# Optimization experiments

Hardware: AMD Instinct MI355X
Metric: run time of the kernel (lower is better)

Reference implementation:

```python
import jax, jax.numpy as jnp
import numpy as np

T = 8          # temporal window (hardcoded '8' in the original)
N = 2048       # num_neurons
S = 8192       # num_synapses per neuron
MAXW = 8.0
UCAPTURE = 10.0 / 128.0
UMINUS = 10.0 / 128.0
USEARCH = 1.0 / 128.0
UBACKOFF = 96.0 / 128.0
UMIN = 4.0 / 128.0


def setup_inputs() -> dict:
    key = jax.random.key(0)
    k1, k2, k3 = jax.random.split(key, 3)
    all_input_spikes = jax.random.randint(k1, (T, N, S), 0, 2, dtype=jnp.int32)
    all_output_spikes = jax.random.randint(k2, (T, N), 0, 2, dtype=jnp.int32)
    W = jax.random.uniform(k3, (N, S), dtype=jnp.float32, minval=-0.5, maxval=8.5)
    return {"all_input_spikes": all_input_spikes,
            "all_output_spikes": all_output_spikes,
            "W": W}


def reference(all_input_spikes, all_output_spikes, W):
    # Clamp weights to [0, 8] (the two torch.where clamps).
    w = jnp.clip(W, 0.0, MAXW)  # [N, S]

    # Spike times encoded as 8 - (spike count over the temporal window).
    in_t = (8 - jnp.sum(all_input_spikes, axis=0)).astype(jnp.int32)        # [N, S]
    out_t = (8 - jnp.sum(all_output_spikes, axis=0)).astype(jnp.int32)[:, None]  # [N, 1]

    wn = w / MAXW
    p_plus = wn * (2.0 - wn)            # Bernoulli prob for fplus
    p_minus = (1.0 - wn) * (1.0 + wn)   # Bernoulli prob for fminus

    rk = jax.random.split(jax.random.key(42), 8)
    dt = w.dtype
    fplus = jax.random.bernoulli(rk[0], p_plus).astype(dt)
    fminus = jax.random.bernoulli(rk[1], p_minus).astype(dt)
    ucap = jax.random.bernoulli(rk[2], UCAPTURE, (N, S)).astype(dt)
    uminus = jax.random.bernoulli(rk[3], UMINUS, (N, S)).astype(dt)
    usearch = jax.random.bernoulli(rk[4], USEARCH, (N, S)).astype(dt)
    ubackoff = jax.random.bernoulli(rk[5], UBACKOFF, (N, S)).astype(dt)
    # umin is sampled independently in each of the four branches
    umin1 = jax.random.bernoulli(rk[6], UMIN, (N, S)).astype(dt)
    k7a, k7b, k7c = jax.random.split(rk[7], 3)
    umin2 = jax.random.bernoulli(k7a, UMIN, (N, S)).astype(dt)
    umin3 = jax.random.bernoulli(k7b, UMIN, (N, S)).astype(dt)
    umin4 = jax.random.bernoulli(k7c, UMIN, (N, S)).astype(dt)

    in_fired = in_t < 8
    out_fired = out_t < 8

    # Branch 1: capture (input at or before output)
    b1 = jnp.where(in_fired & out_fired & (in_t <= out_t),
                   w + ucap * jnp.maximum(fplus, umin1), w)
    # Branch 2: minus (input after output)
    b2 = jnp.where(in_fired & out_fired & (in_t > out_t),
                   b1 - uminus * jnp.maximum(fminus, umin2), b1)
    # Branch 3: search (input fired, output silent)
    b3 = jnp.where(in_fired & (out_t == 8),
                   b2 + usearch * jnp.maximum(fplus, umin3), b2)
    # Branch 4: backoff (input silent, output fired)
    b4 = jnp.where((in_t == 8) & out_fired,
                   b3 - ubackoff * jnp.maximum(fminus, umin4), b3)
    return b4
```

## Files before the change

kernel.cpp:

```cpp
#include <hip/hip_runtime.h>

#define TT 8
#define NN 2048
#define SS 8192
#define MM (NN * SS)

#define TH_CAP10  655360u
#define TH_SEARCH 65536u
#define TH_BACK   6291456u
#define TH_MIN    262144u

#define EPT       8
#define NBLOCKS   (MM / 256 / EPT)

typedef int   __attribute__((ext_vector_type(4))) intx4;
typedef float __attribute__((ext_vector_type(4))) floatx4;
typedef unsigned __attribute__((ext_vector_type(4))) uintx4;

struct Tbl { unsigned v[32]; };

__host__ __device__ __forceinline__ void tf2x32(unsigned k0, unsigned k1,
                                                unsigned x0, unsigned x1,
                                                unsigned& o0, unsigned& o1) {
  const unsigned ks2 = k0 ^ k1 ^ 0x1BD11BDAu;
  x0 += k0; x1 += k1;
#define TFR(r) { x0 += x1; x1 = (x1 << (r)) | (x1 >> (32 - (r))); x1 ^= x0; }
  TFR(13) TFR(15) TFR(26) TFR(6)
  x0 += k1;  x1 += ks2 + 1u;
  TFR(17) TFR(29) TFR(16) TFR(24)
  x0 += ks2; x1 += k0 + 2u;
  TFR(13) TFR(15) TFR(26) TFR(6)
  x0 += k0;  x1 += k1 + 3u;
  TFR(17) TFR(29) TFR(16) TFR(24)
  x0 += k1;  x1 += ks2 + 4u;
  TFR(13) TFR(15) TFR(26) TFR(6)
  x0 += ks2; x1 += k0 + 5u;
#undef TFR
  o0 = x0; o1 = x1;
}

__global__ __launch_bounds__(256) void ModSTDP_58823872086838_kernel(
    const int* __restrict__ inS,
    const int* __restrict__ outS,
    const float* __restrict__ W,
    float* __restrict__ out,
    Tbl tb)
{
  __shared__ __align__(16) unsigned tbl[32];
  if (threadIdx.x < 32) tbl[threadIdx.x] = tb.v[threadIdx.x];
  __syncthreads();

  const unsigned tid  = blockIdx.x * blockDim.x + threadIdx.x;
  const unsigned base = tid * EPT;
  const unsigned n    = base >> 13;

  int osum = 0;
#pragma unroll
  for (int t = 0; t < TT; ++t) osum += outS[t * NN + n];
  const bool outF = osum > 0;

  intx4 s[TT][2];
#pragma unroll
  for (int t = 0; t < TT; ++t) {
    const int* p = inS + (size_t)t * MM + base;
    s[t][0] = *reinterpret_cast<const intx4*>(p);
    s[t][1] = *reinterpret_cast<const intx4*>(p + 4);
  }
  const floatx4 w0 = *reinterpret_cast<const floatx4*>(W + base);
  const floatx4 w1 = *reinterpret_cast<const floatx4*>(W + base + 4);

  int cnt[EPT] = {0, 0, 0, 0, 0, 0, 0, 0};
#pragma unroll
  for (int t = 0; t < TT; ++t) {
#pragma unroll
    for (int e = 0; e < EPT; ++e) cnt[e] += s[t][e >> 2][e & 3];
  }

  float res[EPT];
#pragma unroll
  for (int e = 0; e < EPT; ++e) {
    const unsigned j = base + (unsigned)e;
    const float wraw = (e < 4) ? w0[e & 3] : w1[e & 3];
    const float w = fminf(fmaxf(wraw, 0.0f), 8.0f);
    const int c = cnt[e];
    const bool inF = c > 0;
    const bool active = inF | outF;
    const unsigned idx = inF ? (outF ? ((c >= osum) ? 0u : 1u) : 2u) : 3u;

    const uintx4 r0 = *reinterpret_cast<const uintx4*>(tbl + (idx << 3));
    const uintx4 r1 = *reinterpret_cast<const uintx4*>(tbl + (idx << 3) + 4);
    const unsigned ka0 = r0.x, ka1 = r0.y, kb0 = r0.z, kb1 = r0.w;
    const unsigned kc0 = r1.x, kc1 = r1.y, thB = r1.z;
    const float sgn = __uint_as_float(r1.w);

    const float wn = w * 0.125f;
    const float pp = __fmul_rn(wn, __fsub_rn(2.0f, wn));
    const float pm = __fmul_rn(__fsub_rn(1.0f, wn), __fadd_rn(1.0f, wn));
    const float pA = (idx & 1u) ? pm : pp;

    unsigned a0, a1, b0, b1, c0, c1;
    tf2x32(ka0, ka1, 0u, j, a0, a1);
    const unsigned bitsA = a0 ^ a1;
    const float u = __uint_as_float((bitsA >> 9) | 0x3f800000u) - 1.0f;
    const bool fab = u < pA;

    tf2x32(kb0, kb1, 0u, j, b0, b1);
    const bool gate = (((b0 ^ b1) >> 9) < thB);

    tf2x32(kc0, kc1, 0u, j, c0, c1);
    const bool um = (((c0 ^ c1) >> 9) < TH_MIN);

    const bool doit = active & gate & (fab | um);
    res[e] = doit ? __fadd_rn(w, sgn) : w;
  }

  floatx4 r0, r1;
  r0.x = res[0]; r0.y = res[1]; r0.z = res[2]; r0.w = res[3];
  r1.x = res[4]; r1.y = res[5]; r1.z = res[6]; r1.w = res[7];
  __builtin_nontemporal_store(r0, reinterpret_cast<floatx4*>(out + base));
  __builtin_nontemporal_store(r1, reinterpret_cast<floatx4*>(out + base + 4));
}

extern "C" void kernel_launch(void* const* d_in, const int* in_sizes, int n_in,
                              void* d_out, int out_size, void* d_ws, size_t ws_size,
                              hipStream_t stream) {
  const int*   inS  = (const int*)d_in[0];
  const int*   outS = (const int*)d_in[1];
  const float* W    = (const float*)d_in[2];
  float*       out  = (float*)d_out;

  unsigned kp[20];
  {
    unsigned rk[16];
    for (unsigned i = 0; i < 8; ++i) {
      unsigned o0, o1;
      tf2x32(0u, 42u, 0u, i, o0, o1);
      rk[2 * i] = o0; rk[2 * i + 1] = o1;
    }
    for (int i = 0; i < 14; ++i) kp[i] = rk[i];
    for (unsigned i = 0; i < 3; ++i) {
      unsigned o0, o1;
      tf2x32(rk[14], rk[15], 0u, i, o0, o1);
      kp[14 + 2 * i] = o0; kp[15 + 2 * i] = o1;
    }
  }

  Tbl tb;
  unsigned* v = tb.v;
  v[0] = kp[0];  v[1] = kp[1];  v[2] = kp[4];   v[3] = kp[5];
  v[4] = kp[12]; v[5] = kp[13]; v[6] = TH_CAP10; v[7] = 0x3f800000u;
  v[8] = kp[2];  v[9] = kp[3];  v[10] = kp[6];  v[11] = kp[7];
  v[12] = kp[14]; v[13] = kp[15]; v[14] = TH_CAP10; v[15] = 0xbf800000u;
  v[16] = kp[0]; v[17] = kp[1]; v[18] = kp[8];  v[19] = kp[9];
  v[20] = kp[16]; v[21] = kp[17]; v[22] = TH_SEARCH; v[23] = 0x3f800000u;
  v[24] = kp[2]; v[25] = kp[3]; v[26] = kp[10]; v[27] = kp[11];
  v[28] = kp[18]; v[29] = kp[19]; v[30] = TH_BACK; v[31] = 0xbf800000u;

  ModSTDP_58823872086838_kernel<<<dim3(NBLOCKS), dim3(256), 0, stream>>>(
      inS, outS, W, out, tb);
}
```

Measured before the change: 135.2 us.

## Persistent waves double-buffer spike and weight tiles via global-to-LDS loads

Replaces the one-shot grid of 8-elements-per-thread blocks with a persistent grid of 1024 two-wave blocks. Each wave loops over 256-element tiles, prefetching the next tile's 8 spike planes and weights directly into LDS with global_load_lds while computing the current one, and waits on vmcnt. Each block also precomputes all output-spike sums into shared memory at startup. The goal is to overlap the heavy input streaming with the Threefry RNG compute. The cost is that every block redundantly reads all 2048x8 output spikes, and fewer resident waves limit the memory parallelism available to the loads.

```diff
diff --git a/kernel.cpp b/kernel.cpp
--- a/kernel.cpp
+++ b/kernel.cpp
@@ -10,8 +10,14 @@
 #define TH_BACK   6291456u
 #define TH_MIN    262144u
 
-#define EPT       8
-#define NBLOCKS   (MM / 256 / EPT)
+#define WPB         2
+#define NBLOCKS     1024
+#define TOTAL_WAVES (NBLOCKS * WPB)
+#define EPT         4
+#define TILE_ELEMS  (64 * EPT)
+#define NTILES      (MM / TILE_ELEMS)
+#define ITERS       (NTILES / TOTAL_WAVES)
+#define NPLANES     9
 
 typedef int   __attribute__((ext_vector_type(4))) intx4;
 typedef float __attribute__((ext_vector_type(4))) floatx4;
@@ -39,86 +45,135 @@
   o0 = x0; o1 = x1;
 }
 
-__global__ __launch_bounds__(256) void ModSTDP_58823872086838_kernel(
+#define VMWAIT(N) do {                                                  \
+    asm volatile("s_waitcnt vmcnt(" #N ")" ::: "memory");               \
+    __builtin_amdgcn_sched_barrier(0);                                  \
+  } while (0)
+
+__global__ __launch_bounds__(128) void ModSTDP_58823872086838_kernel(
     const int* __restrict__ inS,
     const int* __restrict__ outS,
     const float* __restrict__ W,
     float* __restrict__ out,
     Tbl tb)
 {
+  __shared__ __align__(16) int ring[WPB][2][NPLANES][TILE_ELEMS];
+  __shared__ unsigned char osum_s[NN];
   __shared__ __align__(16) unsigned tbl[32];
+
   if (threadIdx.x < 32) tbl[threadIdx.x] = tb.v[threadIdx.x];
+  {
+    const int r0 = threadIdx.x * 16;
+    int acc[16];
+#pragma unroll
+    for (int k = 0; k < 16; ++k) acc[k] = 0;
+#pragma unroll
+    for (int t = 0; t < TT; ++t) {
+#pragma unroll
+      for (int k = 0; k < 16; ++k) acc[k] += outS[t * NN + r0 + k];
+    }
+#pragma unroll
+    for (int k = 0; k < 16; ++k) osum_s[r0 + k] = (unsigned char)acc[k];
+  }
   __syncthreads();
 
-  const unsigned tid  = blockIdx.x * blockDim.x + threadIdx.x;
-  const unsigned base = tid * EPT;
-  const unsigned n    = base >> 13;
-
-  int osum = 0;
-#pragma unroll
-  for (int t = 0; t < TT; ++t) osum += outS[t * NN + n];
-  const bool outF = osum > 0;
-
-  intx4 s[TT][2];
-#pragma unroll
-  for (int t = 0; t < TT; ++t) {
-    const int* p = inS + (size_t)t * MM + base;
-    s[t][0] = *reinterpret_cast<const intx4*>(p);
-    s[t][1] = *reinterpret_cast<const intx4*>(p + 4);
+  const unsigned wid  = threadIdx.x >> 6;
+  const unsigned lane = threadIdx.x & 63;
+  unsigned tile = blockIdx.x * WPB + wid;
+
+#define STAGE(T_, B_)                                                        \
+  do {                                                                      \
+    const unsigned eb_ = (T_) * TILE_ELEMS + lane * EPT;                    \
+    _Pragma("unroll")                                                       \
+    for (int t_ = 0; t_ < TT; ++t_) {                                       \
+      const int* src_ = inS + (size_t)t_ * MM + eb_;                        \
+      __builtin_amdgcn_global_load_lds(                                     \
+          (const __attribute__((address_space(1))) void*)src_,              \
+          (__attribute__((address_space(3))) void*)&ring[wid][B_][t_][lane * EPT], \
+          16, 0, 0);                                                        \
+    }                                                                       \
+    const int* wsrc_ = (const int*)W + eb_;                                 \
+    __builtin_amdgcn_global_load_lds(                                       \
+        (const __attribute__((address_space(1))) void*)wsrc_,               \
+        (__attribute__((address_space(3))) void*)&ring[wid][B_][TT][lane * EPT], \
+        16, 0, 0);                                                          \
+  } while (0)
+
+  STAGE(tile, 0);
+
+  unsigned buf = 0;
+#pragma unroll 1
+  for (int it = 0; it < ITERS; ++it) {
+    const unsigned nextTile = tile + TOTAL_WAVES;
+    if (it + 1 < ITERS) {
+      STAGE(nextTile, buf ^ 1);
+      VMWAIT(9);
+    } else {
+      VMWAIT(0);
+    }
+
+    const unsigned ebase = tile * TILE_ELEMS + lane * EPT;
+    const int o = (int)osum_s[tile >> 5];
+    const bool outF = o > 0;
+
+    intx4 sv[TT];
+#pragma unroll
+    for (int t = 0; t < TT; ++t)
+      sv[t] = *(const intx4*)&ring[wid][buf][t][lane * EPT];
+    const floatx4 w4 = *(const floatx4*)&ring[wid][buf][TT][lane * EPT];
+
+    int cnt[EPT] = {0, 0, 0, 0};
+#pragma unroll
+    for (int t = 0; t < TT; ++t) {
+#pragma unroll
+      for (int e = 0; e < EPT; ++e) cnt[e] += sv[t][e];
+    }
+
+    float res[EPT];
+#pragma unroll
+    for (int e = 0; e < EPT; ++e) {
+      const unsigned j = ebase + (unsigned)e;
+      const float w = fminf(fmaxf(w4[e], 0.0f), 8.0f);
+      const int c = cnt[e];
+      const bool inF = c > 0;
+      const bool active = inF | outF;
+      const unsigned idx = inF ? (outF ? ((c >= o) ? 0u : 1u) : 2u) : 3u;
+
+      const uintx4 r0 = *reinterpret_cast<const uintx4*>(tbl + (idx << 3));
+      const uintx4 r1 = *reinterpret_cast<const uintx4*>(tbl + (idx << 3) + 4);
+      const unsigned ka0 = r0.x, ka1 = r0.y, kb0 = r0.z, kb1 = r0.w;
+      const unsigned kc0 = r1.x, kc1 = r1.y, thB = r1.z;
+      const float sgn = __uint_as_float(r1.w);
+
+      const float wn = w * 0.125f;
+      const float pp = __fmul_rn(wn, __fsub_rn(2.0f, wn));
+      const float pm = __fmul_rn(__fsub_rn(1.0f, wn), __fadd_rn(1.0f, wn));
+      const float pA = (idx & 1u) ? pm : pp;
+
+      unsigned a0, a1, b0, b1, c0, c1;
+      tf2x32(ka0, ka1, 0u, j, a0, a1);
+      const unsigned bitsA = a0 ^ a1;
+      const float u = __uint_as_float((bitsA >> 9) | 0x3f800000u) - 1.0f;
+      const bool fab = u < pA;
+
+      tf2x32(kb0, kb1, 0u, j, b0, b1);
+      const bool gate = (((b0 ^ b1) >> 9) < thB);
+
+      tf2x32(kc0, kc1, 0u, j, c0, c1);
+      const bool um = (((c0 ^ c1) >> 9) < TH_MIN);
+
+      const bool doit = active & gate & (fab | um);
+      res[e] = doit ? __fadd_rn(w, sgn) : w;
+    }
+
+    floatx4 r;
+    r.x = res[0]; r.y = res[1]; r.z = res[2]; r.w = res[3];
+    __builtin_nontemporal_store(r, reinterpret_cast<floatx4*>(out + ebase));
+
+    tile = nextTile;
+    buf ^= 1;
   }
-  const floatx4 w0 = *reinterpret_cast<const floatx4*>(W + base);
-  const floatx4 w1 = *reinterpret_cast<const floatx4*>(W + base + 4);
-
-  int cnt[EPT] = {0, 0, 0, 0, 0, 0, 0, 0};
-#pragma unroll
-  for (int t = 0; t < TT; ++t) {
-#pragma unroll
-    for (int e = 0; e < EPT; ++e) cnt[e] += s[t][e >> 2][e & 3];
-  }
-
-  float res[EPT];
-#pragma unroll
-  for (int e = 0; e < EPT; ++e) {
-    const unsigned j = base + (unsigned)e;
-    const float wraw = (e < 4) ? w0[e & 3] : w1[e & 3];
-    const float w = fminf(fmaxf(wraw, 0.0f), 8.0f);
-    const int c = cnt[e];
-    const bool inF = c > 0;
-    const bool active = inF | outF;
-    const unsigned idx = inF ? (outF ? ((c >= osum) ? 0u : 1u) : 2u) : 3u;
-
-    const uintx4 r0 = *reinterpret_cast<const uintx4*>(tbl + (idx << 3));
-    const uintx4 r1 = *reinterpret_cast<const uintx4*>(tbl + (idx << 3) + 4);
-    const unsigned ka0 = r0.x, ka1 = r0.y, kb0 = r0.z, kb1 = r0.w;
-    const unsigned kc0 = r1.x, kc1 = r1.y, thB = r1.z;
-    const float sgn = __uint_as_float(r1.w);
-
-    const float wn = w * 0.125f;
-    const float pp = __fmul_rn(wn, __fsub_rn(2.0f, wn));
-    const float pm = __fmul_rn(__fsub_rn(1.0f, wn), __fadd_rn(1.0f, wn));
-    const float pA = (idx & 1u) ? pm : pp;
-
-    unsigned a0, a1, b0, b1, c0, c1;
-    tf2x32(ka0, ka1, 0u, j, a0, a1);
-    const unsigned bitsA = a0 ^ a1;
-    const float u = __uint_as_float((bitsA >> 9) | 0x3f800000u) - 1.0f;
-    const bool fab = u < pA;
-
-    tf2x32(kb0, kb1, 0u, j, b0, b1);
-    const bool gate = (((b0 ^ b1) >> 9) < thB);
-
-    tf2x32(kc0, kc1, 0u, j, c0, c1);
-    const bool um = (((c0 ^ c1) >> 9) < TH_MIN);
-
-    const bool doit = active & gate & (fab | um);
-    res[e] = doit ? __fadd_rn(w, sgn) : w;
-  }
-
-  floatx4 r0, r1;
-  r0.x = res[0]; r0.y = res[1]; r0.z = res[2]; r0.w = res[3];
-  r1.x = res[4]; r1.y = res[5]; r1.z = res[6]; r1.w = res[7];
-  __builtin_nontemporal_store(r0, reinterpret_cast<floatx4*>(out + base));
-  __builtin_nontemporal_store(r1, reinterpret_cast<floatx4*>(out + base + 4));
+#undef STAGE
 }
 
 extern "C" void kernel_launch(void* const* d_in, const int* in_sizes, int n_in,
@@ -156,6 +211,6 @@
   v[24] = kp[2]; v[25] = kp[3]; v[26] = kp[10]; v[27] = kp[11];
   v[28] = kp[18]; v[29] = kp[19]; v[30] = TH_BACK; v[31] = 0xbf800000u;
 
-  ModSTDP_58823872086838_kernel<<<dim3(NBLOCKS), dim3(256), 0, stream>>>(
+  ModSTDP_58823872086838_kernel<<<dim3(NBLOCKS), dim3(128), 0, stream>>>(
       inS, outS, W, out, tb);
 }
```

Result: slower. 149.0 us (+10.2%).

## Precompute Threefry key schedules on host, use alignbit rotates, 4 elements per thread

Applied to the files above, without the earlier changes.

The host now expands each Threefry key into its full injection schedule (including ks2 and the round constants) and stores it in a larger shared table. The device hash loads these schedules and skips the per-element key-schedule arithmetic. Rotates use the amdgcn alignbit builtin, and only the xor of the two output words is returned. Each thread now handles 4 elements instead of 8, which doubles the grid, raises parallelism and lowers register pressure, at the cost of more LDS reads per element and more blocks loading the table.

```diff
diff --git a/kernel.cpp b/kernel.cpp
--- a/kernel.cpp
+++ b/kernel.cpp
@@ -10,32 +10,58 @@
 #define TH_BACK   6291456u
 #define TH_MIN    262144u
 
-#define EPT       8
-#define NBLOCKS   (MM / 256 / EPT)
+typedef int      __attribute__((ext_vector_type(4))) intx4;
+typedef float    __attribute__((ext_vector_type(4))) floatx4;
+typedef unsigned __attribute__((ext_vector_type(4))) uintx4;
+typedef unsigned __attribute__((ext_vector_type(2))) uintx2;
 
-typedef int   __attribute__((ext_vector_type(4))) intx4;
-typedef float __attribute__((ext_vector_type(4))) floatx4;
-typedef unsigned __attribute__((ext_vector_type(4))) uintx4;
+struct Tbl { unsigned v[160]; };
 
-struct Tbl { unsigned v[32]; };
+#if __has_builtin(__builtin_amdgcn_alignbit)
+#define ROTL(x, r) __builtin_amdgcn_alignbit((x), (x), 32u - (r))
+#else
+#define ROTL(x, r) (((x) << (r)) | ((x) >> (32 - (r))))
+#endif
 
-__host__ __device__ __forceinline__ void tf2x32(unsigned k0, unsigned k1,
-                                                unsigned x0, unsigned x1,
-                                                unsigned& o0, unsigned& o1) {
+#define R4(x0, x1, ra, rb, rc, rd)                   \
+  x0 += x1; x1 = ROTL(x1, ra); x1 ^= x0;             \
+  x0 += x1; x1 = ROTL(x1, rb); x1 ^= x0;             \
+  x0 += x1; x1 = ROTL(x1, rc); x1 ^= x0;             \
+  x0 += x1; x1 = ROTL(x1, rd); x1 ^= x0;
+
+__device__ __forceinline__ unsigned tf_sched(uintx4 s0, uintx4 s1, uintx4 s2,
+                                             unsigned j) {
+  unsigned x0 = s0.x;
+  unsigned x1 = j + s0.y;
+  R4(x0, x1, 13, 15, 26, 6)
+  x0 += s0.z; x1 += s0.w;
+  R4(x0, x1, 17, 29, 16, 24)
+  x0 += s1.x; x1 += s1.y;
+  R4(x0, x1, 13, 15, 26, 6)
+  x0 += s1.z; x1 += s1.w;
+  R4(x0, x1, 17, 29, 16, 24)
+  x0 += s2.x; x1 += s2.y;
+  R4(x0, x1, 13, 15, 26, 6)
+  x0 += s2.z; x1 += s2.w;
+  return x0 ^ x1;
+}
+
+static void tf2x32_host(unsigned k0, unsigned k1, unsigned x0, unsigned x1,
+                        unsigned& o0, unsigned& o1) {
   const unsigned ks2 = k0 ^ k1 ^ 0x1BD11BDAu;
   x0 += k0; x1 += k1;
-#define TFR(r) { x0 += x1; x1 = (x1 << (r)) | (x1 >> (32 - (r))); x1 ^= x0; }
-  TFR(13) TFR(15) TFR(26) TFR(6)
+#define TFRH(r) { x0 += x1; x1 = (x1 << (r)) | (x1 >> (32 - (r))); x1 ^= x0; }
+  TFRH(13) TFRH(15) TFRH(26) TFRH(6)
   x0 += k1;  x1 += ks2 + 1u;
-  TFR(17) TFR(29) TFR(16) TFR(24)
+  TFRH(17) TFRH(29) TFRH(16) TFRH(24)
   x0 += ks2; x1 += k0 + 2u;
-  TFR(13) TFR(15) TFR(26) TFR(6)
+  TFRH(13) TFRH(15) TFRH(26) TFRH(6)
   x0 += k0;  x1 += k1 + 3u;
-  TFR(17) TFR(29) TFR(16) TFR(24)
+  TFRH(17) TFRH(29) TFRH(16) TFRH(24)
   x0 += k1;  x1 += ks2 + 4u;
-  TFR(13) TFR(15) TFR(26) TFR(6)
+  TFRH(13) TFRH(15) TFRH(26) TFRH(6)
   x0 += ks2; x1 += k0 + 5u;
-#undef TFR
+#undef TFRH
   o0 = x0; o1 = x1;
 }
 
@@ -46,12 +72,12 @@
     float* __restrict__ out,
     Tbl tb)
 {
-  __shared__ __align__(16) unsigned tbl[32];
-  if (threadIdx.x < 32) tbl[threadIdx.x] = tb.v[threadIdx.x];
+  __shared__ __align__(16) unsigned tbl[160];
+  if (threadIdx.x < 160) tbl[threadIdx.x] = tb.v[threadIdx.x];
   __syncthreads();
 
   const unsigned tid  = blockIdx.x * blockDim.x + threadIdx.x;
-  const unsigned base = tid * EPT;
+  const unsigned base = tid << 2;
   const unsigned n    = base >> 13;
 
   int osum = 0;
@@ -59,66 +85,63 @@
   for (int t = 0; t < TT; ++t) osum += outS[t * NN + n];
   const bool outF = osum > 0;
 
-  intx4 s[TT][2];
+  const floatx4 w4 = *reinterpret_cast<const floatx4*>(W + base);
+
+  intx4 sp[TT];
 #pragma unroll
-  for (int t = 0; t < TT; ++t) {
-    const int* p = inS + (size_t)t * MM + base;
-    s[t][0] = *reinterpret_cast<const intx4*>(p);
-    s[t][1] = *reinterpret_cast<const intx4*>(p + 4);
-  }
-  const floatx4 w0 = *reinterpret_cast<const floatx4*>(W + base);
-  const floatx4 w1 = *reinterpret_cast<const floatx4*>(W + base + 4);
+  for (int t = 0; t < TT; ++t)
+    sp[t] = *reinterpret_cast<const intx4*>(inS + (size_t)t * MM + base);
 
-  int cnt[EPT] = {0, 0, 0, 0, 0, 0, 0, 0};
+  int cnt[4] = {0, 0, 0, 0};
 #pragma unroll
   for (int t = 0; t < TT; ++t) {
 #pragma unroll
-    for (int e = 0; e < EPT; ++e) cnt[e] += s[t][e >> 2][e & 3];
+    for (int e = 0; e < 4; ++e) cnt[e] += sp[t][e];
   }
 
-  float res[EPT];
+  float res[4];
 #pragma unroll
-  for (int e = 0; e < EPT; ++e) {
+  for (int e = 0; e < 4; ++e) {
     const unsigned j = base + (unsigned)e;
-    const float wraw = (e < 4) ? w0[e & 3] : w1[e & 3];
-    const float w = fminf(fmaxf(wraw, 0.0f), 8.0f);
+    const float w = fminf(fmaxf(w4[e], 0.0f), 8.0f);
     const int c = cnt[e];
     const bool inF = c > 0;
     const bool active = inF | outF;
     const unsigned idx = inF ? (outF ? ((c >= osum) ? 0u : 1u) : 2u) : 3u;
-
-    const uintx4 r0 = *reinterpret_cast<const uintx4*>(tbl + (idx << 3));
-    const uintx4 r1 = *reinterpret_cast<const uintx4*>(tbl + (idx << 3) + 4);
-    const unsigned ka0 = r0.x, ka1 = r0.y, kb0 = r0.z, kb1 = r0.w;
-    const unsigned kc0 = r1.x, kc1 = r1.y, thB = r1.z;
-    const float sgn = __uint_as_float(r1.w);
+    const unsigned* row = tbl + idx * 40u;
 
     const float wn = w * 0.125f;
     const float pp = __fmul_rn(wn, __fsub_rn(2.0f, wn));
     const float pm = __fmul_rn(__fsub_rn(1.0f, wn), __fadd_rn(1.0f, wn));
     const float pA = (idx & 1u) ? pm : pp;
 
-    unsigned a0, a1, b0, b1, c0, c1;
-    tf2x32(ka0, ka1, 0u, j, a0, a1);
-    const unsigned bitsA = a0 ^ a1;
+    uintx4 s0 = *reinterpret_cast<const uintx4*>(row);
+    uintx4 s1 = *reinterpret_cast<const uintx4*>(row + 4);
+    uintx4 s2 = *reinterpret_cast<const uintx4*>(row + 8);
+    const unsigned bitsA = tf_sched(s0, s1, s2, j);
     const float u = __uint_as_float((bitsA >> 9) | 0x3f800000u) - 1.0f;
     const bool fab = u < pA;
 
-    tf2x32(kb0, kb1, 0u, j, b0, b1);
-    const bool gate = (((b0 ^ b1) >> 9) < thB);
+    s0 = *reinterpret_cast<const uintx4*>(row + 12);
+    s1 = *reinterpret_cast<const uintx4*>(row + 16);
+    s2 = *reinterpret_cast<const uintx4*>(row + 20);
+    const uintx2 tc = *reinterpret_cast<const uintx2*>(row + 36);
+    const unsigned bitsB = tf_sched(s0, s1, s2, j);
+    const bool gate = (bitsB >> 9) < tc.x;
 
-    tf2x32(kc0, kc1, 0u, j, c0, c1);
-    const bool um = (((c0 ^ c1) >> 9) < TH_MIN);
+    s0 = *reinterpret_cast<const uintx4*>(row + 24);
+    s1 = *reinterpret_cast<const uintx4*>(row + 28);
+    s2 = *reinterpret_cast<const uintx4*>(row + 32);
+    const unsigned bitsC = tf_sched(s0, s1, s2, j);
+    const bool um = (bitsC >> 9) < TH_MIN;
 
     const bool doit = active & gate & (fab | um);
-    res[e] = doit ? __fadd_rn(w, sgn) : w;
+    res[e] = doit ? __fadd_rn(w, __uint_as_float(tc.y)) : w;
   }
 
-  floatx4 r0, r1;
-  r0.x = res[0]; r0.y = res[1]; r0.z = res[2]; r0.w = res[3];
-  r1.x = res[4]; r1.y = res[5]; r1.z = res[6]; r1.w = res[7];
-  __builtin_nontemporal_store(r0, reinterpret_cast<floatx4*>(out + base));
-  __builtin_nontemporal_store(r1, reinterpret_cast<floatx4*>(out + base + 4));
+  floatx4 r;
+  r.x = res[0]; r.y = res[1]; r.z = res[2]; r.w = res[3];
+  __builtin_nontemporal_store(r, reinterpret_cast<floatx4*>(out + base));
 }
 
 extern "C" void kernel_launch(void* const* d_in, const int* in_sizes, int n_in,
@@ -134,28 +157,42 @@
     unsigned rk[16];
     for (unsigned i = 0; i < 8; ++i) {
       unsigned o0, o1;
-      tf2x32(0u, 42u, 0u, i, o0, o1);
+      tf2x32_host(0u, 42u, 0u, i, o0, o1);
       rk[2 * i] = o0; rk[2 * i + 1] = o1;
     }
     for (int i = 0; i < 14; ++i) kp[i] = rk[i];
     for (unsigned i = 0; i < 3; ++i) {
       unsigned o0, o1;
-      tf2x32(rk[14], rk[15], 0u, i, o0, o1);
+      tf2x32_host(rk[14], rk[15], 0u, i, o0, o1);
       kp[14 + 2 * i] = o0; kp[15 + 2 * i] = o1;
     }
   }
 
+  auto emit = [](unsigned* d, unsigned K0, unsigned K1) {
+    const unsigned ks2 = K0 ^ K1 ^ 0x1BD11BDAu;
+    d[0] = K0;  d[1] = K1;       d[2]  = K1;  d[3]  = ks2 + 1u;
+    d[4] = ks2; d[5] = K0 + 2u;  d[6]  = K0;  d[7]  = K1 + 3u;
+    d[8] = K1;  d[9] = ks2 + 4u; d[10] = ks2; d[11] = K0 + 5u;
+  };
+
   Tbl tb;
-  unsigned* v = tb.v;
-  v[0] = kp[0];  v[1] = kp[1];  v[2] = kp[4];   v[3] = kp[5];
-  v[4] = kp[12]; v[5] = kp[13]; v[6] = TH_CAP10; v[7] = 0x3f800000u;
-  v[8] = kp[2];  v[9] = kp[3];  v[10] = kp[6];  v[11] = kp[7];
-  v[12] = kp[14]; v[13] = kp[15]; v[14] = TH_CAP10; v[15] = 0xbf800000u;
-  v[16] = kp[0]; v[17] = kp[1]; v[18] = kp[8];  v[19] = kp[9];
-  v[20] = kp[16]; v[21] = kp[17]; v[22] = TH_SEARCH; v[23] = 0x3f800000u;
-  v[24] = kp[2]; v[25] = kp[3]; v[26] = kp[10]; v[27] = kp[11];
-  v[28] = kp[18]; v[29] = kp[19]; v[30] = TH_BACK; v[31] = 0xbf800000u;
+  const unsigned rowspec[4][8] = {
+    {0, 1, 4, 5, 12, 13, TH_CAP10,  0x3f800000u},
+    {2, 3, 6, 7, 14, 15, TH_CAP10,  0xbf800000u},
+    {0, 1, 8, 9, 16, 17, TH_SEARCH, 0x3f800000u},
+    {2, 3, 10, 11, 18, 19, TH_BACK, 0xbf800000u},
+  };
+  for (int r = 0; r < 4; ++r) {
+    unsigned* d = tb.v + r * 40;
+    emit(d,      kp[rowspec[r][0]], kp[rowspec[r][1]]);
+    emit(d + 12, kp[rowspec[r][2]], kp[rowspec[r][3]]);
+    emit(d + 24, kp[rowspec[r][4]], kp[rowspec[r][5]]);
+    d[36] = rowspec[r][6];
+    d[37] = rowspec[r][7];
+    d[38] = 0; d[39] = 0;
+  }
 
-  ModSTDP_58823872086838_kernel<<<dim3(NBLOCKS), dim3(256), 0, stream>>>(
-      inS, outS, W, out, tb);
+  const int threads = MM / 4;
+  dim3 block(256), grid(threads / 256);
+  ModSTDP_58823872086838_kernel<<<grid, block, 0, stream>>>(inS, outS, W, out, tb);
 }
```

Result: faster. 130.6 us (-3.4%).
